# Optimization experiments

Measured on AMD Instinct MI355X. Metric: run time of the kernel, lower is better.

The kernel has to match this reference:

```python
import jax, jax.numpy as jnp
import numpy as np
from jax import lax

MIN_VALUE = 0.0
MAX_VALUE = 1.0

# 5-point Laplacian stencil kernel, OIHW layout
_LAP_KERNEL = jnp.array([[0.0, 1.0, 0.0],
                         [1.0, -4.0, 1.0],
                         [0.0, 1.0, 0.0]], dtype=jnp.float32).reshape(1, 1, 3, 3)


def _laplacian(u):
    # u: [B, 1, H, W], zero-padded 3x3 stencil (SAME)
    return lax.conv_general_dilated(
        u, _LAP_KERNEL, window_strides=(1, 1), padding='SAME',
        dimension_numbers=('NCHW', 'OIHW', 'NCHW'))


def _step(u, params):
    # Fisher-Kolmogorov reaction-diffusion step:
    #   diff = D * laplacian(u) + rho * u * (1 - u)
    D = params[:, 0:1]    # [B,1,H,W]
    rho = params[:, 1:2]  # [B,1,H,W]
    return D * _laplacian(u) + rho * u * (1.0 - u)


def setup_inputs() -> dict:
    key = jax.random.key(0)
    k1, k2, k3 = jax.random.split(key, 3)
    B, H, W = 32, 256, 256
    u = jax.random.uniform(k1, (B, 1, H, W), dtype=jnp.float32)
    params = jax.random.uniform(k2, (B, 2, H, W), dtype=jnp.float32)
    t = jax.random.randint(k3, (B,), 0, 32, dtype=jnp.int32)
    return {"u": u, "params": params, "t": t}


def reference(u, params, t):
    # Original: for step in range(max(t)): u[t>step] += step(u[t>step], params[t>step]); clip(u).
    # The step is per-sample local, so masked gather/scatter == predicated full update.
    max_duration = int(jnp.max(t))  # static trip count

    def body(step, u):
        mask = (t > step).astype(u.dtype)[:, None, None, None]  # [B,1,1,1]
        u = u + mask * _step(u, params)
        return jnp.clip(u, MIN_VALUE, MAX_VALUE)

    return lax.fori_loop(0, max_duration, body, u)
```

## Files before the change

kernel.cpp:

```cpp
#include <hip/hip_runtime.h>

#define HH 256
#define WW 256
#define PLANE (HH * WW)
#define CORE 32
#define HALO 31
#define NW 16
#define RPW 6

__device__ __forceinline__ float dpp_shfl_up1(float x) {
    return __int_as_float(__builtin_amdgcn_update_dpp(
        0, __float_as_int(x), 0x138 , 0xf, 0xf, true));
}
__device__ __forceinline__ float dpp_shfl_dn1(float x) {
    return __int_as_float(__builtin_amdgcn_update_dpp(
        0, __float_as_int(x), 0x130 , 0xf, 0xf, true));
}

__global__ __launch_bounds__(1024, 4)
void rd_single_kernel(const float* __restrict__ uin,
                      const float* __restrict__ params,
                      const int* __restrict__ t,
                      float* __restrict__ uout)
{
    __shared__ float4 vt[2][NW][64];
    __shared__ float4 vb[2][NW][64];

    const int blk   = blockIdx.x;
    const int b     = blk >> 3;
    const int strip = blk & 7;
    const int r0    = strip * CORE;
    const int w     = threadIdx.x >> 6;
    const int lane  = threadIdx.x & 63;
    const int c0    = lane << 2;

    int ls = t[b];
    if (ls > 31) ls = 31;
    if (ls < 0)  ls = 0;

    int d_min;
    if (w <= 4)       d_min = 26 - 6 * w;
    else if (w >= 11) d_min = 6 * w - 62;
    else              d_min = 0;
    int my_steps = ls - d_min;
    if (my_steps < 0) my_steps = 0;

    const int growbase = r0 - HALO + RPW * w;
    const size_t ubase = (size_t)b * PLANE;
    const size_t pbase = (size_t)b * 2 * PLANE;

    float u[RPW][4], pD[RPW][4], pR[RPW][4];

    #pragma unroll
    for (int dr = 0; dr < RPW; ++dr) {
        const int grow = growbase + dr;
        const bool inimg = (grow >= 0) && (grow < HH);
        int dist = 0;
        if (grow < r0)                 dist = r0 - grow;
        else if (grow > r0 + CORE - 1) dist = grow - (r0 + CORE - 1);
        const bool needU = inimg && (dist <= ls);
        const bool needP = inimg && (dist < ls);

        if (needU) {
            const float4 uu = *reinterpret_cast<const float4*>(uin + ubase + (size_t)grow * WW + c0);
            u[dr][0] = uu.x; u[dr][1] = uu.y; u[dr][2] = uu.z; u[dr][3] = uu.w;
        } else {
            u[dr][0] = u[dr][1] = u[dr][2] = u[dr][3] = 0.f;
        }
        if (needP) {
            const float4 dd = *reinterpret_cast<const float4*>(params + pbase + (size_t)grow * WW + c0);
            const float4 rr = *reinterpret_cast<const float4*>(params + pbase + PLANE + (size_t)grow * WW + c0);
            pD[dr][0] = dd.x; pD[dr][1] = dd.y; pD[dr][2] = dd.z; pD[dr][3] = dd.w;
            pR[dr][0] = rr.x; pR[dr][1] = rr.y; pR[dr][2] = rr.z; pR[dr][3] = rr.w;
        } else {
            pD[dr][0] = pD[dr][1] = pD[dr][2] = pD[dr][3] = 0.f;
            pR[dr][0] = pR[dr][1] = pR[dr][2] = pR[dr][3] = 0.f;
        }
    }

    if (ls > 0) {
        vt[0][w][lane] = make_float4(u[0][0], u[0][1], u[0][2], u[0][3]);
        vb[0][w][lane] = make_float4(u[RPW-1][0], u[RPW-1][1], u[RPW-1][2], u[RPW-1][3]);

        for (int s = 0; s < ls; ++s) {
            __syncthreads();
            if (s < my_steps) {
                const int cur = s & 1;

                float upr[4] = {0.f, 0.f, 0.f, 0.f};
                float dnr[4] = {0.f, 0.f, 0.f, 0.f};
                if (w > 0)      { float4 v = vb[cur][w-1][lane]; upr[0]=v.x; upr[1]=v.y; upr[2]=v.z; upr[3]=v.w; }
                if (w < NW - 1) { float4 v = vt[cur][w+1][lane]; dnr[0]=v.x; dnr[1]=v.y; dnr[2]=v.z; dnr[3]=v.w; }

                float up_old[4];
                #pragma unroll
                for (int dr = 0; dr < RPW; ++dr) {
                    const float lf = dpp_shfl_up1(u[dr][3]);
                    const float rt = dpp_shfl_dn1(u[dr][0]);

                    float old[4], un[4];
                    #pragma unroll
                    for (int c = 0; c < 4; ++c) old[c] = u[dr][c];

                    #pragma unroll
                    for (int c = 0; c < 4; ++c) {
                        const float upv = dr ? up_old[c] : upr[c];
                        const float dnv = (dr < RPW - 1) ? u[dr+1][c] : dnr[c];
                        const float lv  = c ? old[c-1] : lf;
                        const float rv  = (c < 3) ? old[c+1] : rt;
                        const float uc  = old[c];
                        const float s4  = (upv + dnv) + (lv + rv);
                        const float lap = fmaf(-4.0f, uc, s4);
                        const float g   = fmaf(-uc, uc, uc);
                        const float a   = fmaf(pD[dr][c], lap, uc);
                        const float nv  = fmaf(pR[dr][c], g, a);
                        un[c] = __builtin_amdgcn_fmed3f(nv, 0.0f, 1.0f);
                    }
                    #pragma unroll
                    for (int c = 0; c < 4; ++c) { u[dr][c] = un[c]; up_old[c] = old[c]; }
                }

                const int nxt = cur ^ 1;
                vt[nxt][w][lane] = make_float4(u[0][0], u[0][1], u[0][2], u[0][3]);
                vb[nxt][w][lane] = make_float4(u[RPW-1][0], u[RPW-1][1], u[RPW-1][2], u[RPW-1][3]);
            }
        }
    }

    #pragma unroll
    for (int dr = 0; dr < RPW; ++dr) {
        const int grow = growbase + dr;
        if (grow >= r0 && grow < r0 + CORE) {
            *reinterpret_cast<float4*>(uout + ubase + (size_t)grow * WW + c0) =
                make_float4(u[dr][0], u[dr][1], u[dr][2], u[dr][3]);
        }
    }
}

extern "C" void kernel_launch(void* const* d_in, const int* in_sizes, int n_in,
                              void* d_out, int out_size, void* d_ws, size_t ws_size,
                              hipStream_t stream) {
    (void)in_sizes; (void)n_in; (void)out_size; (void)d_ws; (void)ws_size;
    const float* u      = (const float*)d_in[0];
    const float* params = (const float*)d_in[1];
    const int*   t      = (const int*)d_in[2];
    float*       out    = (float*)d_out;

    rd_single_kernel<<<dim3(256), dim3(1024), 0, stream>>>(u, params, t, out);
}
```

Measured before the change: 54.48 us.

## Split time steps into two launches with smaller halo and two-step temporal blocking

Replaces the single launch with a 31-row halo by two launches of up to 16 and 15 steps, each using a 16-row halo and a global workspace between rounds. Each wave now owns 4 rows plus 2 ghost rows on each side, exchanging 2 rows through shared memory every 2 steps, which halves the number of barriers. This cuts redundant halo computation and halo loads. The cost is a second launch and a round trip of the intermediate field through global memory.

```diff
diff --git a/kernel.cpp b/kernel.cpp
--- a/kernel.cpp
+++ b/kernel.cpp
@@ -4,9 +4,9 @@
 #define WW 256
 #define PLANE (HH * WW)
 #define CORE 32
-#define HALO 31
+#define HALO 16
 #define NW 16
-#define RPW 6
+#define KSTEP 2
 
 __device__ __forceinline__ float dpp_shfl_up1(float x) {
     return __int_as_float(__builtin_amdgcn_update_dpp(
@@ -17,14 +17,47 @@
         0, __float_as_int(x), 0x130 , 0xf, 0xf, true));
 }
 
+template<int LO, int HI>
+__device__ __forceinline__ void step_range(float (&u)[8][4],
+                                           const float (&pD)[6][4],
+                                           const float (&pR)[6][4]) {
+    float carry[4];
+    #pragma unroll
+    for (int c = 0; c < 4; ++c) carry[c] = u[LO - 1][c];
+    #pragma unroll
+    for (int r = LO; r <= HI; ++r) {
+        const float lf = dpp_shfl_up1(u[r][3]);
+        const float rt = dpp_shfl_dn1(u[r][0]);
+        float old[4];
+        #pragma unroll
+        for (int c = 0; c < 4; ++c) old[c] = u[r][c];
+        #pragma unroll
+        for (int c = 0; c < 4; ++c) {
+            const float upv = carry[c];
+            const float dnv = u[r + 1][c];
+            const float lv  = c ? old[c - 1] : lf;
+            const float rv  = (c < 3) ? old[c + 1] : rt;
+            const float uc  = old[c];
+            const float s4  = (upv + dnv) + (lv + rv);
+            const float lap = fmaf(-4.0f, uc, s4);
+            const float g   = fmaf(-uc, uc, uc);
+            const float a   = fmaf(pD[r - 1][c], lap, uc);
+            const float nv  = fmaf(pR[r - 1][c], g, a);
+            u[r][c] = __builtin_amdgcn_fmed3f(nv, 0.0f, 1.0f);
+        }
+        #pragma unroll
+        for (int c = 0; c < 4; ++c) carry[c] = old[c];
+    }
+}
+
 __global__ __launch_bounds__(1024, 4)
-void rd_single_kernel(const float* __restrict__ uin,
-                      const float* __restrict__ params,
-                      const int* __restrict__ t,
-                      float* __restrict__ uout)
+void rd_round_kernel(const float* __restrict__ uin,
+                     const float* __restrict__ params,
+                     const int* __restrict__ t,
+                     float* __restrict__ uout,
+                     int base, int ktot)
 {
-    __shared__ float4 vt[2][NW][64];
-    __shared__ float4 vb[2][NW][64];
+    __shared__ float4 pub[2][NW][4][64];
 
     const int blk   = blockIdx.x;
     const int b     = blk >> 3;
@@ -34,105 +67,86 @@
     const int lane  = threadIdx.x & 63;
     const int c0    = lane << 2;
 
-    int ls = t[b];
-    if (ls > 31) ls = 31;
-    if (ls < 0)  ls = 0;
+    int ls = t[b] - base;
+    ls = ls < 0 ? 0 : (ls > ktot ? ktot : ls);
 
-    int d_min;
-    if (w <= 4)       d_min = 26 - 6 * w;
-    else if (w >= 11) d_min = 6 * w - 62;
-    else              d_min = 0;
+    int tg = 16 - (4 * w + 3), bg = 4 * w - 47;
+    int d_min = tg > bg ? tg : bg;
+    if (d_min < 0) d_min = 0;
     int my_steps = ls - d_min;
     if (my_steps < 0) my_steps = 0;
 
-    const int growbase = r0 - HALO + RPW * w;
+    const int base_row = r0 - HALO + 4 * w;
     const size_t ubase = (size_t)b * PLANE;
     const size_t pbase = (size_t)b * 2 * PLANE;
 
-    float u[RPW][4], pD[RPW][4], pR[RPW][4];
+    float u[8][4], pD[6][4], pR[6][4];
 
     #pragma unroll
-    for (int dr = 0; dr < RPW; ++dr) {
-        const int grow = growbase + dr;
-        const bool inimg = (grow >= 0) && (grow < HH);
+    for (int L = 0; L < 8; ++L)
+        #pragma unroll
+        for (int c = 0; c < 4; ++c) u[L][c] = 0.f;
+
+    #pragma unroll
+    for (int L = 2; L <= 5; ++L) {
+        const int grow = base_row + (L - 2);
         int dist = 0;
         if (grow < r0)                 dist = r0 - grow;
         else if (grow > r0 + CORE - 1) dist = grow - (r0 + CORE - 1);
-        const bool needU = inimg && (dist <= ls);
-        const bool needP = inimg && (dist < ls);
-
-        if (needU) {
+        if (grow >= 0 && grow < HH && dist <= ls) {
             const float4 uu = *reinterpret_cast<const float4*>(uin + ubase + (size_t)grow * WW + c0);
-            u[dr][0] = uu.x; u[dr][1] = uu.y; u[dr][2] = uu.z; u[dr][3] = uu.w;
-        } else {
-            u[dr][0] = u[dr][1] = u[dr][2] = u[dr][3] = 0.f;
+            u[L][0] = uu.x; u[L][1] = uu.y; u[L][2] = uu.z; u[L][3] = uu.w;
         }
-        if (needP) {
+    }
+    #pragma unroll
+    for (int L = 1; L <= 6; ++L) {
+        const int grow = base_row + (L - 2);
+        int dist = 0;
+        if (grow < r0)                 dist = r0 - grow;
+        else if (grow > r0 + CORE - 1) dist = grow - (r0 + CORE - 1);
+        if (grow >= 0 && grow < HH && dist < ls) {
             const float4 dd = *reinterpret_cast<const float4*>(params + pbase + (size_t)grow * WW + c0);
             const float4 rr = *reinterpret_cast<const float4*>(params + pbase + PLANE + (size_t)grow * WW + c0);
-            pD[dr][0] = dd.x; pD[dr][1] = dd.y; pD[dr][2] = dd.z; pD[dr][3] = dd.w;
-            pR[dr][0] = rr.x; pR[dr][1] = rr.y; pR[dr][2] = rr.z; pR[dr][3] = rr.w;
+            pD[L-1][0] = dd.x; pD[L-1][1] = dd.y; pD[L-1][2] = dd.z; pD[L-1][3] = dd.w;
+            pR[L-1][0] = rr.x; pR[L-1][1] = rr.y; pR[L-1][2] = rr.z; pR[L-1][3] = rr.w;
         } else {
-            pD[dr][0] = pD[dr][1] = pD[dr][2] = pD[dr][3] = 0.f;
-            pR[dr][0] = pR[dr][1] = pR[dr][2] = pR[dr][3] = 0.f;
+            pD[L-1][0] = pD[L-1][1] = pD[L-1][2] = pD[L-1][3] = 0.f;
+            pR[L-1][0] = pR[L-1][1] = pR[L-1][2] = pR[L-1][3] = 0.f;
         }
     }
 
-    if (ls > 0) {
-        vt[0][w][lane] = make_float4(u[0][0], u[0][1], u[0][2], u[0][3]);
-        vb[0][w][lane] = make_float4(u[RPW-1][0], u[RPW-1][1], u[RPW-1][2], u[RPW-1][3]);
+    int bufi = 0;
+    for (int s0 = 0; s0 < ls; s0 += KSTEP) {
+        pub[bufi][w][0][lane] = make_float4(u[2][0], u[2][1], u[2][2], u[2][3]);
+        pub[bufi][w][1][lane] = make_float4(u[3][0], u[3][1], u[3][2], u[3][3]);
+        pub[bufi][w][2][lane] = make_float4(u[4][0], u[4][1], u[4][2], u[4][3]);
+        pub[bufi][w][3][lane] = make_float4(u[5][0], u[5][1], u[5][2], u[5][3]);
+        __syncthreads();
+        if (w > 0) {
+            const float4 a = pub[bufi][w-1][2][lane];
+            const float4 q = pub[bufi][w-1][3][lane];
+            u[0][0]=a.x; u[0][1]=a.y; u[0][2]=a.z; u[0][3]=a.w;
+            u[1][0]=q.x; u[1][1]=q.y; u[1][2]=q.z; u[1][3]=q.w;
+        }
+        if (w < NW - 1) {
+            const float4 a = pub[bufi][w+1][0][lane];
+            const float4 q = pub[bufi][w+1][1][lane];
+            u[6][0]=a.x; u[6][1]=a.y; u[6][2]=a.z; u[6][3]=a.w;
+            u[7][0]=q.x; u[7][1]=q.y; u[7][2]=q.z; u[7][3]=q.w;
+        }
+        bufi ^= 1;
 
-        for (int s = 0; s < ls; ++s) {
-            __syncthreads();
-            if (s < my_steps) {
-                const int cur = s & 1;
-
-                float upr[4] = {0.f, 0.f, 0.f, 0.f};
-                float dnr[4] = {0.f, 0.f, 0.f, 0.f};
-                if (w > 0)      { float4 v = vb[cur][w-1][lane]; upr[0]=v.x; upr[1]=v.y; upr[2]=v.z; upr[3]=v.w; }
-                if (w < NW - 1) { float4 v = vt[cur][w+1][lane]; dnr[0]=v.x; dnr[1]=v.y; dnr[2]=v.z; dnr[3]=v.w; }
-
-                float up_old[4];
-                #pragma unroll
-                for (int dr = 0; dr < RPW; ++dr) {
-                    const float lf = dpp_shfl_up1(u[dr][3]);
-                    const float rt = dpp_shfl_dn1(u[dr][0]);
-
-                    float old[4], un[4];
-                    #pragma unroll
-                    for (int c = 0; c < 4; ++c) old[c] = u[dr][c];
-
-                    #pragma unroll
-                    for (int c = 0; c < 4; ++c) {
-                        const float upv = dr ? up_old[c] : upr[c];
-                        const float dnv = (dr < RPW - 1) ? u[dr+1][c] : dnr[c];
-                        const float lv  = c ? old[c-1] : lf;
-                        const float rv  = (c < 3) ? old[c+1] : rt;
-                        const float uc  = old[c];
-                        const float s4  = (upv + dnv) + (lv + rv);
-                        const float lap = fmaf(-4.0f, uc, s4);
-                        const float g   = fmaf(-uc, uc, uc);
-                        const float a   = fmaf(pD[dr][c], lap, uc);
-                        const float nv  = fmaf(pR[dr][c], g, a);
-                        un[c] = __builtin_amdgcn_fmed3f(nv, 0.0f, 1.0f);
-                    }
-                    #pragma unroll
-                    for (int c = 0; c < 4; ++c) { u[dr][c] = un[c]; up_old[c] = old[c]; }
-                }
-
-                const int nxt = cur ^ 1;
-                vt[nxt][w][lane] = make_float4(u[0][0], u[0][1], u[0][2], u[0][3]);
-                vb[nxt][w][lane] = make_float4(u[RPW-1][0], u[RPW-1][1], u[RPW-1][2], u[RPW-1][3]);
-            }
-        }
+        const int jend = my_steps - s0;
+        if (jend >= 1) step_range<1, 6>(u, pD, pR);
+        if (jend >= 2) step_range<2, 5>(u, pD, pR);
     }
 
     #pragma unroll
-    for (int dr = 0; dr < RPW; ++dr) {
-        const int grow = growbase + dr;
+    for (int L = 2; L <= 5; ++L) {
+        const int grow = base_row + (L - 2);
         if (grow >= r0 && grow < r0 + CORE) {
             *reinterpret_cast<float4*>(uout + ubase + (size_t)grow * WW + c0) =
-                make_float4(u[dr][0], u[dr][1], u[dr][2], u[dr][3]);
+                make_float4(u[L][0], u[L][1], u[L][2], u[L][3]);
         }
     }
 }
@@ -140,11 +154,14 @@
 extern "C" void kernel_launch(void* const* d_in, const int* in_sizes, int n_in,
                               void* d_out, int out_size, void* d_ws, size_t ws_size,
                               hipStream_t stream) {
-    (void)in_sizes; (void)n_in; (void)out_size; (void)d_ws; (void)ws_size;
+    (void)in_sizes; (void)n_in; (void)out_size; (void)ws_size;
     const float* u      = (const float*)d_in[0];
     const float* params = (const float*)d_in[1];
     const int*   t      = (const int*)d_in[2];
     float*       out    = (float*)d_out;
+    float*       ws     = (float*)d_ws;
 
-    rd_single_kernel<<<dim3(256), dim3(1024), 0, stream>>>(u, params, t, out);
+    const dim3 grid(256), block(1024);
+    rd_round_kernel<<<grid, block, 0, stream>>>(u,  params, t, ws,  0,  16);
+    rd_round_kernel<<<grid, block, 0, stream>>>(ws, params, t, out, 16, 15);
 }
```

After: 56.80 us. +4.3%, slower.
